# Optimization experiments

Measured on AMD Instinct MI355X. Metric: run time of the kernel, lower is better.

Reference implementation:

```python
import jax, jax.numpy as jnp
import numpy as np

K = 5    # reassembly kernel size (kernel_size)
UP = 2   # upsample factor (up_factor)


def setup_inputs() -> dict:
    key = jax.random.key(0)
    k1, k2 = jax.random.split(key)
    B, C, H, W = 8, 256, 64, 64
    inp = jax.random.normal(k1, (B, C, H, W), dtype=jnp.float32)
    # per-pixel reassembly weights: up^2 * k^2 channels at low resolution
    km = jax.random.uniform(k2, (B, UP * UP * K * K, H, W), dtype=jnp.float32)
    return {"input": inp, "kernel_map": km}


def _carafe(x, km):
    # x:  [B, C, H, W]
    # km: [B, up^2 * k^2, H, W]
    B, C, H, W = x.shape
    pad = K // 2
    xp = jnp.pad(x, ((0, 0), (0, 0), (pad, pad), (pad, pad)))  # zero boundary
    # Extract kxk neighborhoods: fixed 25-iteration loop over kernel offsets
    # patches: [B, C, k*k, H, W]
    patches = jnp.stack(
        [xp[:, :, i:i + H, j:j + W] for i in range(K) for j in range(K)],
        axis=2,
    )
    # weights per sub-pixel output position: [B, up^2, k*k, H, W]
    w = km.reshape(B, UP * UP, K * K, H, W)
    # content-aware weighted reassembly
    out = jnp.einsum('bckhw,bukhw->buchw', patches, w)  # [B, up^2, C, H, W]
    # pixel-shuffle: sub-pixel index u = i*UP + j -> (h*UP+i, w*UP+j)
    out = out.reshape(B, UP, UP, C, H, W)
    out = out.transpose(0, 3, 4, 1, 5, 2)  # [B, C, H, UP, W, UP]
    return out.reshape(B, C, H * UP, W * UP)


def reference(input, kernel_map):
    return _carafe(input, kernel_map)
```

## Files before the change

### kernel.cpp

```cpp
#include <hip/hip_runtime.h>

namespace {
constexpr int Bn = 8, Cn = 256, Hn = 64, Wn = 64;
constexpr int Kk = 5, PAD = 2, KMC = 100;
constexpr int CSPLIT = 2;
constexpr int CPB = Cn / CSPLIT;
constexpr int NWG = Hn * Bn * CSPLIT;
constexpr int NXCD = 8;
constexpr int CHUNK = NWG / NXCD;
}

__global__ __launch_bounds__(256, 2) void carafe_fwd(
    const float* __restrict__ x,
    const float* __restrict__ km,
    float* __restrict__ out)
{
    const int wg   = blockIdx.x;
    const int orig = (wg & (NXCD - 1)) * CHUNK + (wg >> 3);
    const int cz   = orig & 1;
    const int h    = (orig >> 1) & (Hn - 1);
    const int b    = orig >> 7;

    const int tid = threadIdx.x;
    const int wv  = tid >> 6;
    const int w   = tid & 63;

    __shared__ __align__(16) float xs[4][Kk][68][4];

    if (w < Kk * 4) {
        const int r  = w >> 2;
        const int hc = w & 3;
        const int wp = (hc < 2) ? hc : 64 + hc;
        #pragma unroll
        for (int k = 0; k < 4; ++k) xs[wv][r][wp][k] = 0.0f;
    }

    float wreg[KMC];
    {
        const float* kmp = km + (((size_t)b * KMC) * Hn + h) * Wn + w;
        #pragma unroll
        for (int ch = 0; ch < KMC; ++ch)
            wreg[ch] = kmp[(size_t)ch * (Hn * Wn)];
    }

    const float* xb = x + (size_t)b * Cn * Hn * Wn;
    float* ob       = out + (size_t)b * Cn * (2 * Hn) * (2 * Wn);

    for (int cb = 0; cb < CPB / 16; ++cb) {
        const int c0 = cz * CPB + cb * 16 + wv * 4;

        #pragma unroll
        for (int r = 0; r < Kk; ++r) {
            const int hr = h - PAD + r;
            float4 v;
            if (hr >= 0 && hr < Hn) {
                const float* xr = xb + ((size_t)c0 * Hn + hr) * Wn + w;
                v.x = xr[0 * Hn * Wn];
                v.y = xr[1 * Hn * Wn];
                v.z = xr[2 * Hn * Wn];
                v.w = xr[3 * Hn * Wn];
            } else {
                v = make_float4(0.f, 0.f, 0.f, 0.f);
            }
            *(float4*)(&xs[wv][r][w + PAD][0]) = v;
        }

        asm volatile("s_waitcnt lgkmcnt(0)" ::: "memory");

        float acc[4][4] = {};
        #pragma unroll
        for (int kh = 0; kh < Kk; ++kh) {
            #pragma unroll
            for (int kw = 0; kw < Kk; ++kw) {
                const float4 tap = *(const float4*)(&xs[wv][kh][w + kw][0]);
                const int t = kh * Kk + kw;
                #pragma unroll
                for (int u = 0; u < 4; ++u) {
                    const float wt = wreg[u * 25 + t];
                    acc[0][u] += tap.x * wt;
                    acc[1][u] += tap.y * wt;
                    acc[2][u] += tap.z * wt;
                    acc[3][u] += tap.w * wt;
                }
            }
        }

        asm volatile("" ::: "memory");

        #pragma unroll
        for (int k = 0; k < 4; ++k) {
            #pragma unroll
            for (int i = 0; i < 2; ++i) {
                float2 o2 = make_float2(acc[k][2 * i + 0], acc[k][2 * i + 1]);
                *(float2*)(&ob[((size_t)(c0 + k) * (2 * Hn) + (2 * h + i)) *
                                   (2 * Wn) + 2 * w]) = o2;
            }
        }
    }
}

extern "C" void kernel_launch(void* const* d_in, const int* in_sizes, int n_in,
                              void* d_out, int out_size, void* d_ws, size_t ws_size,
                              hipStream_t stream)
{
    const float* x  = (const float*)d_in[0];
    const float* km = (const float*)d_in[1];
    float* out      = (float*)d_out;

    dim3 grid(NWG);
    carafe_fwd<<<grid, 256, 0, stream>>>(x, km, out);
}
```

Measured before the change: 211.1 us.

## Double-buffer input tiles via async global_load_lds to overlap loads with compute

Swaps the register-staged global loads followed by LDS stores for direct global-to-LDS loads (global_load_lds), and double-buffers the per-wave LDS slab. The next channel block is prefetched while the current one is computed, with hand-tuned vmcnt waits. Out-of-range rows are redirected to a dummy LDS buffer, so the zeroed padding stays intact. It aims to hide global load latency and remove VGPR round trips. In exchange it doubles LDS use and relies on fragile vmcnt counts that also include the wreg and output-store memory operations.

```diff
diff --git a/kernel.cpp b/kernel.cpp
--- a/kernel.cpp
+++ b/kernel.cpp
@@ -8,6 +8,8 @@
 constexpr int NWG = Hn * Bn * CSPLIT;
 constexpr int NXCD = 8;
 constexpr int CHUNK = NWG / NXCD;
+constexpr int HW = Hn * Wn;
+constexpr int NCB = CPB / 16;
 }
 
 __global__ __launch_bounds__(256, 2) void carafe_fwd(
@@ -25,54 +27,67 @@
     const int wv  = tid >> 6;
     const int w   = tid & 63;
 
-    __shared__ __align__(16) float xs[4][Kk][68][4];
+    __shared__ __align__(16) float xs[4][2][Kk][68][4];
+    __shared__ float dummy[64];
 
-    if (w < Kk * 4) {
-        const int r  = w >> 2;
-        const int hc = w & 3;
-        const int wp = (hc < 2) ? hc : 64 + hc;
-        #pragma unroll
-        for (int k = 0; k < 4; ++k) xs[wv][r][wp][k] = 0.0f;
+    {
+        float* slab = &xs[wv][0][0][0][0];
+        for (int i = w; i < 2 * Kk * 68 * 4; i += 64) slab[i] = 0.0f;
     }
+    asm volatile("s_waitcnt lgkmcnt(0)" ::: "memory");
 
     float wreg[KMC];
     {
         const float* kmp = km + (((size_t)b * KMC) * Hn + h) * Wn + w;
         #pragma unroll
         for (int ch = 0; ch < KMC; ++ch)
-            wreg[ch] = kmp[(size_t)ch * (Hn * Wn)];
+            wreg[ch] = kmp[(size_t)ch * HW];
     }
 
-    const float* xb = x + (size_t)b * Cn * Hn * Wn;
+    const float* xb = x + (size_t)b * Cn * HW;
     float* ob       = out + (size_t)b * Cn * (2 * Hn) * (2 * Wn);
 
-    for (int cb = 0; cb < CPB / 16; ++cb) {
+    const int sl_ch = w & 3;
+    const int sl_cl = w >> 2;
+
+    auto STAGE = [&](int bi, int c0s) {
+        #pragma unroll
+        for (int r = 0; r < Kk; ++r) {
+            const int hr  = h - PAD + r;
+            const int hrc = hr < 0 ? 0 : (hr >= Hn ? Hn - 1 : hr);
+            const bool valid = (hr == hrc);
+            const float* srow =
+                xb + (size_t)(c0s + sl_ch) * HW + hrc * Wn + sl_cl;
+            #pragma unroll
+            for (int q = 0; q < 4; ++q) {
+                float* d = valid ? &xs[wv][bi][r][2 + 16 * q][0] : &dummy[0];
+                __builtin_amdgcn_global_load_lds(
+                    (const __attribute__((address_space(1))) void*)(srow + 16 * q),
+                    (__attribute__((address_space(3))) void*)d, 4, 0, 0);
+            }
+        }
+    };
+
+    STAGE(0, cz * CPB + wv * 4);
+
+    #pragma unroll 1
+    for (int cb = 0; cb < NCB; ++cb) {
         const int c0 = cz * CPB + cb * 16 + wv * 4;
 
-        #pragma unroll
-        for (int r = 0; r < Kk; ++r) {
-            const int hr = h - PAD + r;
-            float4 v;
-            if (hr >= 0 && hr < Hn) {
-                const float* xr = xb + ((size_t)c0 * Hn + hr) * Wn + w;
-                v.x = xr[0 * Hn * Wn];
-                v.y = xr[1 * Hn * Wn];
-                v.z = xr[2 * Hn * Wn];
-                v.w = xr[3 * Hn * Wn];
-            } else {
-                v = make_float4(0.f, 0.f, 0.f, 0.f);
-            }
-            *(float4*)(&xs[wv][r][w + PAD][0]) = v;
-        }
+        if (cb + 1 < NCB)
+            STAGE((cb + 1) & 1, c0 + 16);
 
-        asm volatile("s_waitcnt lgkmcnt(0)" ::: "memory");
+        if (cb == 0)            asm volatile("s_waitcnt vmcnt(20)" ::: "memory");
+        else if (cb + 1 < NCB)  asm volatile("s_waitcnt vmcnt(28)" ::: "memory");
+        else                    asm volatile("s_waitcnt vmcnt(8)"  ::: "memory");
 
+        const int bi = cb & 1;
         float acc[4][4] = {};
         #pragma unroll
         for (int kh = 0; kh < Kk; ++kh) {
             #pragma unroll
             for (int kw = 0; kw < Kk; ++kw) {
-                const float4 tap = *(const float4*)(&xs[wv][kh][w + kw][0]);
+                const float4 tap = *(const float4*)(&xs[wv][bi][kh][w + kw][0]);
                 const int t = kh * Kk + kw;
                 #pragma unroll
                 for (int u = 0; u < 4; ++u) {
@@ -84,8 +99,6 @@
                 }
             }
         }
-
-        asm volatile("" ::: "memory");
 
         #pragma unroll
         for (int k = 0; k < 4; ++k) {
```

Result: faster. 198.6 us (-5.9%).
